# Kernel tuning notes

Hardware: AMD Instinct MI355X
Metric: run time of the kernel (lower is better)

The kernel has to match this reference:

```python
import jax, jax.numpy as jnp
import numpy as np

C = 320        # in_channels == inner_dim (n_heads*d_head = 8*40)
HEADS = 8
DH = 40
CTX = 768
FF_INNER = 1280  # 4*C
G = 32         # GroupNorm groups


def _ln(x, w, b, eps=1e-5):
    m = x.mean(-1, keepdims=True)
    v = ((x - m) ** 2).mean(-1, keepdims=True)
    return (x - m) * jax.lax.rsqrt(v + eps) * w + b


def _attn(q, k, v, heads, scale):
    # faithful to source: split last dim as (d h) -> head index is fastest
    B, Lq, D = q.shape
    Lk = k.shape[1]
    dh = D // heads
    q = q.reshape(B, Lq, dh, heads).transpose(0, 3, 1, 2)  # b h i d
    k = k.reshape(B, Lk, dh, heads).transpose(0, 3, 1, 2)  # b h j d
    v = v.reshape(B, Lk, dh, heads).transpose(0, 3, 1, 2)
    sim = jnp.einsum('bhid,bhjd->bhij', q, k) * scale
    w = jax.nn.softmax(sim, axis=-1)
    o = jnp.einsum('bhij,bhjd->bhid', w, v)
    # merge as (h d): head index is slowest on output (matches source)
    return o.transpose(0, 2, 1, 3).reshape(B, Lq, heads * dh)


def setup_inputs() -> dict:
    key = jax.random.key(0)
    ks = jax.random.split(key, 20)
    n = lambda i, shape: jax.random.normal(ks[i], shape, jnp.float32) * 0.02
    z = lambda d: jnp.zeros((d,), jnp.float32)
    o = lambda d: jnp.ones((d,), jnp.float32)
    return dict(
        x=jax.random.normal(ks[0], (1, C, 64, 64), jnp.float32),
        context=jax.random.normal(ks[1], (1, 77, CTX), jnp.float32),
        gn_w=o(C), gn_b=z(C),
        w_in=n(2, (C, C)), b_in=z(C),
        ln1_w=o(C), ln1_b=z(C),
        wq1=n(3, (C, C)), wk1=n(4, (C, C)), wv1=n(5, (C, C)),
        wo1=n(6, (C, C)), bo1=z(C),
        ln2_w=o(C), ln2_b=z(C),
        wq2=n(7, (C, C)), wk2=n(8, (CTX, C)), wv2=n(9, (CTX, C)),
        wo2=n(10, (C, C)), bo2=z(C),
        ln3_w=o(C), ln3_b=z(C),
        wff1=n(11, (C, 2 * FF_INNER)), bff1=z(2 * FF_INNER),
        wff2=n(12, (FF_INNER, C)), bff2=z(C),
        w_out=n(13, (C, C)), b_out=z(C),
    )


def reference(x, context, gn_w, gn_b, w_in, b_in,
              ln1_w, ln1_b, wq1, wk1, wv1, wo1, bo1,
              ln2_w, ln2_b, wq2, wk2, wv2, wo2, bo2,
              ln3_w, ln3_b, wff1, bff1, wff2, bff2,
              w_out, b_out):
    B, Cc, H, W = x.shape
    scale = DH ** (-0.5)
    x_in = x
    # GroupNorm(32, eps=1e-6)
    g = x.reshape(B, G, Cc // G, H, W)
    m = g.mean((2, 3, 4), keepdims=True)
    v = ((g - m) ** 2).mean((2, 3, 4), keepdims=True)
    h = ((g - m) * jax.lax.rsqrt(v + 1e-6)).reshape(B, Cc, H, W)
    h = h * gn_w[None, :, None, None] + gn_b[None, :, None, None]
    # 1x1 conv in_proj
    h = jnp.einsum('bchw,co->bohw', h, w_in) + b_in[None, :, None, None]
    # b c h w -> b (h w) c
    t = h.transpose(0, 2, 3, 1).reshape(B, H * W, C)
    # --- transformer block (depth=1) ---
    # attn_1: self-attn; NOTE source applies k/v proj to the QUERY projection
    hn = _ln(t, ln1_w, ln1_b)
    q = hn @ wq1
    k = q @ wk1
    vv = q @ wv1
    t = t + (_attn(q, k, vv, HEADS, scale) @ wo1 + bo1)
    # attn_2: cross-attn with context
    hn = _ln(t, ln2_w, ln2_b)
    q = hn @ wq2
    k = context @ wk2
    vv = context @ wv2
    t = t + (_attn(q, k, vv, HEADS, scale) @ wo2 + bo2)
    # GEGLU feed-forward
    hn = _ln(t, ln3_w, ln3_b)
    p = hn @ wff1 + bff1
    a, gate = p[..., :FF_INNER], p[..., FF_INNER:]
    t = t + ((a * jax.nn.gelu(gate, approximate=False)) @ wff2 + bff2)
    # b (h w) c -> b c h w
    s = t.reshape(B, H, W, C).transpose(0, 3, 1, 2)
    out = jnp.einsum('bchw,co->bohw', s, w_out) + b_out[None, :, None, None]
    return out + x_in
```

## Files before the change

### kernel.cpp

```cpp
#include <hip/hip_runtime.h>
#include <hip/hip_bf16.h>
#include <math.h>

#define CCH 320
#define NHEADS 8
#define DH 40
#define HW 4096
#define FFI 1280

typedef __bf16 bf16x8 __attribute__((ext_vector_type(8)));
typedef unsigned short u16x8 __attribute__((ext_vector_type(8)));
typedef short s16x4 __attribute__((ext_vector_type(4)));
typedef float f32x4 __attribute__((ext_vector_type(4)));
typedef unsigned int u32x4 __attribute__((ext_vector_type(4)));

__device__ inline unsigned short f2bf(float f) {
    __hip_bfloat16 h = __float2bfloat16(f);
    return __builtin_bit_cast(unsigned short, h);
}
__device__ inline unsigned pk2bf(float a, float b) {
#if __has_builtin(__builtin_amdgcn_cvt_pk_bf16_f32)
    typedef __bf16 bf16x2 __attribute__((ext_vector_type(2)));
    bf16x2 r = __builtin_amdgcn_cvt_pk_bf16_f32(a, b);
    return __builtin_bit_cast(unsigned, r);
#else
    return (unsigned)f2bf(a) | ((unsigned)f2bf(b) << 16);
#endif
}
__device__ inline float bf2f(unsigned short u) {
    return __builtin_bit_cast(float, ((unsigned)u) << 16);
}
__device__ inline bf16x8 ldfrag(const unsigned short* p) {
    u16x8 raw = *reinterpret_cast<const u16x8*>(p);
    return __builtin_bit_cast(bf16x8, raw);
}
__device__ inline s16x4 pk2frag(unsigned a, unsigned b) {
    unsigned long long v = (unsigned long long)a | ((unsigned long long)b << 32);
    return __builtin_bit_cast(s16x4, v);
}

__device__ inline float ex2(float x) {
#if __has_builtin(__builtin_amdgcn_exp2f)
    return __builtin_amdgcn_exp2f(x);
#else
    return exp2f(x);
#endif
}
__device__ inline float fast_rcp(float x) {
#if __has_builtin(__builtin_amdgcn_rcpf)
    return __builtin_amdgcn_rcpf(x);
#else
    return 1.f / x;
#endif
}
__device__ inline float fast_gelu(float x) {
    float z = fabsf(x) * 0.70710678118654752f;
    float t = fast_rcp(fmaf(0.3275911f, z, 1.f));
    float poly = fmaf(fmaf(fmaf(fmaf(1.061405429f, t, -1.453152027f), t,
                               1.421413741f), t, -0.284496736f), t,
                      0.254829592f) * t;
    float e = ex2(z * z * -1.4426950408889634f);
    float erfz = 1.f - poly * e;
    float s = copysignf(erfz, x);
    return 0.5f * x * (1.f + s);
}

__global__ __launch_bounds__(256) void prep_w2(
    const float* __restrict__ w_in, const float* __restrict__ wq1,
    const float* __restrict__ wk1, const float* __restrict__ wv1,
    const float* __restrict__ wo1, const float* __restrict__ wq2,
    const float* __restrict__ wo2, const float* __restrict__ w_out,
    const float* __restrict__ wff1, const float* __restrict__ wff2,
    const float* __restrict__ wk2, const float* __restrict__ wv2,
    unsigned short* __restrict__ Wt) {
    __shared__ float tile[64][65];
    const int b = blockIdx.x, tid = threadIdx.x;
    const float* src;
    int K, stride, dstoff, k0, n0;
    bool glu = false;
    if (b < 200) {
        int m = b / 25, t = b % 25;
        k0 = (t / 5) * 64; n0 = (t % 5) * 64;
        K = 320; stride = 320; dstoff = m * 102400;
        src = (m == 0) ? w_in : (m == 1) ? wq1 : (m == 2) ? wk1 :
              (m == 3) ? wv1 : (m == 4) ? wo1 : (m == 5) ? wq2 :
              (m == 6) ? wo2 : w_out;
    } else if (b < 300) {
        int t = b - 200;
        k0 = (t / 5) * 64; n0 = (t % 5) * 64;
        K = 1280; stride = 320; dstoff = 1638400; src = wff2;
    } else if (b < 500) {
        int t = b - 300;
        k0 = (t / 40) * 64; n0 = (t % 40) * 64;
        K = 320; stride = 2560; dstoff = 819200; src = wff1; glu = true;
    } else if (b < 560) {
        int t = b - 500;
        k0 = (t / 5) * 64; n0 = (t % 5) * 64;
        K = 768; stride = 320; dstoff = 2048000; src = wk2;
    } else {
        int t = b - 560;
        k0 = (t / 5) * 64; n0 = (t % 5) * 64;
        K = 768; stride = 320; dstoff = 2048000 + 245760; src = wv2;
    }
#pragma unroll
    for (int i = 0; i < 16; ++i) {
        int idx = tid + i * 256;
        int r = idx >> 6, cn = idx & 63;
        int scol = glu ? ((n0 >> 1) + (cn >> 1) + (cn & 1) * FFI) : (n0 + cn);
        tile[r][cn] = src[(size_t)(k0 + r) * stride + scol];
    }
    __syncthreads();
#pragma unroll
    for (int i = 0; i < 16; ++i) {
        int idx = tid + i * 256;
        int cl = idx >> 6, cr = idx & 63;
        Wt[dstoff + (size_t)(n0 + cl) * K + k0 + cr] = f2bf(tile[cr][cl]);
    }
}

__global__ void pack_ctx(const float* __restrict__ ctx,
                         unsigned short* __restrict__ D) {
    int idx = blockIdx.x * 256 + threadIdx.x;
    int row = idx / 768, col = idx - row * 768;
    float v = (row < 77) ? ctx[row * 768 + col] : 0.f;
    D[idx] = f2bf(v);
}

__global__ __launch_bounds__(256) void gn_stats(const float* __restrict__ X,
                                                float2* __restrict__ part) {
    __shared__ float s1[256], s2[256];
    const int b = blockIdx.x, tid = threadIdx.x;
    const float* xg = X + b * 5120;
    float s = 0.f, sq = 0.f;
#pragma unroll
    for (int i = 0; i < 20; ++i) { float v = xg[tid + i * 256]; s += v; sq += v * v; }
    s1[tid] = s; s2[tid] = sq; __syncthreads();
    for (int off = 128; off > 0; off >>= 1) {
        if (tid < off) { s1[tid] += s1[tid + off]; s2[tid] += s2[tid + off]; }
        __syncthreads();
    }
    if (tid == 0) part[b] = make_float2(s1[0], s2[0]);
}

__global__ __launch_bounds__(256) void gn_apply(const float* __restrict__ X,
                                                const float2* __restrict__ part,
                                                const float* __restrict__ w,
                                                const float* __restrict__ b,
                                                unsigned short* __restrict__ Y) {
    __shared__ float tile[64][65];
    __shared__ float gm[32], gr[32];
    const int tid = threadIdx.x;
    const int hw0 = blockIdx.x * 64, c0 = blockIdx.y * 64;
    if (tid < 32) {
        float s = 0.f, sq = 0.f;
#pragma unroll
        for (int i = 0; i < 8; ++i) { float2 p = part[tid * 8 + i]; s += p.x; sq += p.y; }
        float mean = s * (1.f / 40960.f);
        float var  = sq * (1.f / 40960.f) - mean * mean;
        gm[tid] = mean; gr[tid] = rsqrtf(var + 1e-6f);
    }
#pragma unroll
    for (int i = 0; i < 16; ++i) {
        int idx = tid + i * 256;
        int r = idx >> 6, col = idx & 63;
        tile[r][col] = X[(size_t)(c0 + r) * HW + hw0 + col];
    }
    __syncthreads();
#pragma unroll
    for (int i = 0; i < 16; ++i) {
        int idx = tid + i * 256;
        int hwl = idx >> 6, cl = idx & 63;
        int c = c0 + cl, g = c / 10;
        float v = (tile[cl][hwl] - gm[g]) * gr[g] * w[c] + b[c];
        Y[(size_t)(hw0 + hwl) * CCH + c] = f2bf(v);
    }
}

__global__ __launch_bounds__(256) void ln_kernel(const float* __restrict__ X,
                                                 const float* __restrict__ w,
                                                 const float* __restrict__ b,
                                                 unsigned short* __restrict__ Y) {
    const int row  = blockIdx.x * 4 + (threadIdx.x >> 6);
    const int lane = threadIdx.x & 63;
    const float* xr = X + row * CCH;
    const float4 a = *(const float4*)(xr + lane * 4);
    const float  e = xr[256 + lane];
    float v[5] = {a.x, a.y, a.z, a.w, e};
    float s = 0.f, sq = 0.f;
#pragma unroll
    for (int i = 0; i < 5; ++i) { s += v[i]; sq += v[i] * v[i]; }
#pragma unroll
    for (int off = 32; off > 0; off >>= 1) {
        s  += __shfl_xor(s, off, 64);
        sq += __shfl_xor(sq, off, 64);
    }
    const float mean = s * (1.f / 320.f);
    const float var  = sq * (1.f / 320.f) - mean * mean;
    const float rstd = rsqrtf(var + 1e-5f);
    unsigned short* yr = Y + row * CCH;
    const float4 w4 = *(const float4*)(w + lane * 4);
    const float4 b4 = *(const float4*)(b + lane * 4);
    float r0 = (v[0] - mean) * rstd * w4.x + b4.x;
    float r1 = (v[1] - mean) * rstd * w4.y + b4.y;
    float r2 = (v[2] - mean) * rstd * w4.z + b4.z;
    float r3 = (v[3] - mean) * rstd * w4.w + b4.w;
    *(uint2*)(yr + lane * 4) = make_uint2(pk2bf(r0, r1), pk2bf(r2, r3));
    int ct = 256 + lane;
    yr[ct] = f2bf((v[4] - mean) * rstd * w[ct] + b[ct]);
}

template <int MT, int K>
__global__ __launch_bounds__(256) void gemm4(
    const unsigned short* __restrict__ A,
    const unsigned short* __restrict__ Bt,
    const float* __restrict__ bias,
    const float* __restrict__ res,
    void* __restrict__ Cout, void* __restrict__ Cout2,
    int N, int mode, float scale) {
    constexpr int NCH = K / 64;
    __shared__ __align__(16) unsigned short Ab[2][MT * 16 * 64];
    __shared__ __align__(16) unsigned short Bb[2][64 * 64];
    const int tid  = threadIdx.x;
    const int wave = tid >> 6, lane = tid & 63;
    const int quad = lane >> 4, c = lane & 15;
    const int m0 = blockIdx.y * (MT * 16);
    const int bn = blockIdx.x;

    f32x4 acc[MT];
#pragma unroll
    for (int i = 0; i < MT; ++i) acc[i] = (f32x4){0.f, 0.f, 0.f, 0.f};

    const unsigned short* aslab = A + (size_t)m0 * K;
    const unsigned short* bslab = Bt + (size_t)(bn * 64) * K;

    constexpr int ITA = MT * 16 * 8 / 256;
    int arow[ITA], aoff[ITA];
#pragma unroll
    for (int i = 0; i < ITA; ++i) {
        int idx = tid + i * 256;
        arow[i] = idx >> 3;
        int g = idx & 7;
        aoff[i] = arow[i] * 64 + ((g ^ (arow[i] & 7)) * 8);
    }
    int brow[2], boff[2];
#pragma unroll
    for (int i = 0; i < 2; ++i) {
        int idx = tid + i * 256;
        brow[i] = idx >> 3;
        int g = idx & 7;
        boff[i] = brow[i] * 64 + ((g ^ (brow[i] & 7)) * 8);
    }
    const int ag = (tid & 7) * 8;

    {
        u16x8 ra[ITA], rb[2];
#pragma unroll
        for (int i = 0; i < ITA; ++i)
            ra[i] = *(const u16x8*)(aslab + (size_t)arow[i] * K + ag);
#pragma unroll
        for (int i = 0; i < 2; ++i)
            rb[i] = *(const u16x8*)(bslab + (size_t)brow[i] * K + ag);
#pragma unroll
        for (int i = 0; i < ITA; ++i) *(u16x8*)&Ab[0][aoff[i]] = ra[i];
#pragma unroll
        for (int i = 0; i < 2; ++i) *(u16x8*)&Bb[0][boff[i]] = rb[i];
    }
    __syncthreads();

    const int swz0 = (quad ^ (c & 7)) * 8;
    const int swz1 = ((quad + 4) ^ (c & 7)) * 8;
#pragma unroll
    for (int ch = 0; ch < NCH; ++ch) {
        const int buf = ch & 1;
        u16x8 ra[ITA], rb[2];
        if (ch + 1 < NCH) {
            const int kb = (ch + 1) * 64;
#pragma unroll
            for (int i = 0; i < ITA; ++i)
                ra[i] = *(const u16x8*)(aslab + (size_t)arow[i] * K + kb + ag);
#pragma unroll
            for (int i = 0; i < 2; ++i)
                rb[i] = *(const u16x8*)(bslab + (size_t)brow[i] * K + kb + ag);
        }
        bf16x8 b0 = ldfrag(&Bb[buf][(wave * 16 + c) * 64 + swz0]);
        bf16x8 b1 = ldfrag(&Bb[buf][(wave * 16 + c) * 64 + swz1]);
#pragma unroll
        for (int mt = 0; mt < MT; ++mt) {
            bf16x8 a0 = ldfrag(&Ab[buf][(mt * 16 + c) * 64 + swz0]);
            bf16x8 a1 = ldfrag(&Ab[buf][(mt * 16 + c) * 64 + swz1]);
            acc[mt] = __builtin_amdgcn_mfma_f32_16x16x32_bf16(a0, b0, acc[mt], 0, 0, 0);
            acc[mt] = __builtin_amdgcn_mfma_f32_16x16x32_bf16(a1, b1, acc[mt], 0, 0, 0);
        }
        if (ch + 1 < NCH) {
            const int nb = buf ^ 1;
#pragma unroll
            for (int i = 0; i < ITA; ++i) *(u16x8*)&Ab[nb][aoff[i]] = ra[i];
#pragma unroll
            for (int i = 0; i < 2; ++i) *(u16x8*)&Bb[nb][boff[i]] = rb[i];
        }
        __syncthreads();
    }

    const int col = bn * 64 + wave * 16 + c;
    float bval = 0.f;
    if (bias) bval = (mode == 5) ? bias[(col >> 1) + (col & 1) * FFI] : bias[col];

    if (mode == 9) {
#pragma unroll
        for (int mt = 0; mt < MT; ++mt) {
            const int row0 = m0 + mt * 16 + quad * 4;
            float4 xv = *(const float4*)(res + (size_t)col * HW + row0);
            float4 ov;
            ov.x = acc[mt][0] + bval + xv.x;
            ov.y = acc[mt][1] + bval + xv.y;
            ov.z = acc[mt][2] + bval + xv.z;
            ov.w = acc[mt][3] + bval + xv.w;
            *(float4*)((float*)Cout + (size_t)col * HW + row0) = ov;
        }
        return;
    }
#pragma unroll
    for (int mt = 0; mt < MT; ++mt) {
#pragma unroll
        for (int r = 0; r < 4; ++r) {
            const int row = m0 + mt * 16 + quad * 4 + r;
            float v = acc[mt][r];
            if (mode == 0) {
                v += bval;
                if (res) v += res[(size_t)row * N + col];
                ((float*)Cout)[(size_t)row * N + col] = v;
            } else if (mode == 2) {
                int h = col & 7, d = col >> 3;
                ((unsigned short*)Cout)[(((size_t)h << 12) + row) * 64 + d] = f2bf(v * scale);
                if (d < 24)
                    ((unsigned short*)Cout)[(((size_t)h << 12) + row) * 64 + 40 + d] = 0;
            } else if (mode == 4) {
                ((unsigned short*)Cout)[(size_t)row * N + col] =
                    f2bf(v + bval + res[(size_t)row * N + col]);
            } else if (mode == 5) {
                v += bval;
                float other = __shfl_xor(v, 1, 64);
                if ((c & 1) == 0) {
                    float g = fast_gelu(other);
                    ((unsigned short*)Cout)[(size_t)row * FFI + (col >> 1)] = f2bf(v * g);
                }
            } else if (mode == 6) {
                ((unsigned short*)Cout)[(size_t)row * N + col] = f2bf(v);
                int h = col & 7, d = col >> 3;
                ((unsigned short*)Cout2)[(((size_t)h << 12) + row) * 64 + d] = f2bf(v * scale);
                if (d < 24)
                    ((unsigned short*)Cout2)[(((size_t)h << 12) + row) * 64 + 40 + d] = 0;
            } else if (mode == 7) {
                if (col < 320) {
                    int h = col & 7, d = col >> 3;
                    ((unsigned short*)Cout)[(((size_t)h << 12) + row) * 64 + d] = f2bf(v);
                    if (d < 24)
                        ((unsigned short*)Cout)[(((size_t)h << 12) + row) * 64 + 40 + d] = 0;
                } else {
                    int c2 = col - 320;
                    int h = c2 & 7, d = c2 >> 3;
                    ((unsigned short*)Cout2)[(((size_t)(h * 48 + d)) << 12) + row] = f2bf(v);
                    if (d < 8)
                        ((unsigned short*)Cout2)[(((size_t)(h * 48 + 40 + d)) << 12) + row] =
                            (d == 0) ? (unsigned short)0x3F80 : (unsigned short)0;
                }
            } else {
                if (col < 320) {
                    int h = col & 7, d = col >> 3;
                    ((unsigned short*)Cout)[(((size_t)h << 7) + row) * 64 + d] = f2bf(v);
                    if (d < 24)
                        ((unsigned short*)Cout)[(((size_t)h << 7) + row) * 64 + 40 + d] = 0;
                } else {
                    int c2 = col - 320;
                    int h = c2 & 7, d = c2 >> 3;
                    ((unsigned short*)Cout2)[(size_t)(h * 48 + d) * 128 + row] = f2bf(v);
                    if (d < 8)
                        ((unsigned short*)Cout2)[(size_t)(h * 48 + 40 + d) * 128 + row] =
                            (d == 0) ? (unsigned short)0x3F80 : (unsigned short)0;
                }
            }
        }
    }
}

template <int TILES, bool MASK, bool FINAL>
__global__ __launch_bounds__(256) void attn8(
    const unsigned short* __restrict__ Qp,
    const unsigned short* __restrict__ Kp,
    const unsigned short* __restrict__ Vt,
    float* __restrict__ pO, float* __restrict__ pL,
    unsigned short* __restrict__ Ofin,
    int Lk, int Lkp) {
    __shared__ __align__(16) unsigned short Kb[2][64 * 64];
    __shared__ __align__(16) unsigned short Vb[2][48 * 64];
    const int tid  = threadIdx.x;
    const int wave = tid >> 6, lane = tid & 63;
    const int quad = lane >> 4, c = lane & 15;
    const int id  = blockIdx.x;
    const int h   = id & 7;
    const int qt  = (id >> 3) & 31;
    const int seg = id >> 8;
    const int q0  = qt * 128 + wave * 32;

    const unsigned short* qbaseA = Qp + ((((size_t)h << 12) + q0 + c) << 6) + quad * 8;
    const bf16x8 bQA0 = ldfrag(qbaseA);
    const bf16x8 bQA1 = ldfrag(qbaseA + 32);
    const bf16x8 bQB0 = ldfrag(qbaseA + 1024);
    const bf16x8 bQB1 = ldfrag(qbaseA + 1024 + 32);

    f32x4 oA[3], oB[3];
#pragma unroll
    for (int i = 0; i < 3; ++i) {
        oA[i] = (f32x4){0.f, 0.f, 0.f, 0.f};
        oB[i] = (f32x4){0.f, 0.f, 0.f, 0.f};
    }

    const int kt0 = seg * TILES;
    const unsigned short* kglob = Kp + (((size_t)h * Lkp + kt0 * 64) << 6);
    const unsigned short* vglob = Vt + ((size_t)h * 48) * Lkp + kt0 * 64;

    const int r0 = lane >> 3;
    const int g  = lane & 7;
    int ldsoff[4];
    const unsigned short* gptr0[4];
#pragma unroll
    for (int i = 0; i < 4; ++i) {
        int s = wave + 4 * i;
        if (s < 8) {
            int row = s * 8 + r0;
            ldsoff[i] = row * 64 + (g ^ (row & 7)) * 8;
            gptr0[i]  = kglob + (size_t)row * 64 + g * 8;
        } else if (s < 14) {
            int d = (s - 8) * 8 + r0;
            ldsoff[i] = d * 64 + (g ^ (d & 7)) * 8;
            gptr0[i]  = vglob + (size_t)d * Lkp + g * 8;
        } else {
            ldsoff[i] = 0; gptr0[i] = nullptr;
        }
    }
    const bool isK[4] = {(wave + 0) < 8, (wave + 4) < 8, (wave + 8) < 8, (wave + 12) < 8};
    const bool act[4] = {true, true, true, (wave + 12) < 14};

    {
        u16x8 st[4];
#pragma unroll
        for (int i = 0; i < 4; ++i)
            if (act[i]) st[i] = *(const u16x8*)(gptr0[i]);
#pragma unroll
        for (int i = 0; i < 4; ++i)
            if (act[i]) {
                unsigned short* lp = isK[i] ? &Kb[0][ldsoff[i]] : &Vb[0][ldsoff[i]];
                *(u16x8*)lp = st[i];
            }
    }
    __syncthreads();

#pragma unroll
    for (int t = 0; t < TILES; ++t) {
        const int b = t & 1;
        u16x8 st[4];
        if (t + 1 < TILES) {
            const int kb = (t + 1) * 64;
#pragma unroll
            for (int i = 0; i < 4; ++i)
                if (act[i]) {
                    const unsigned short* gp =
                        isK[i] ? (gptr0[i] + (size_t)kb * 64) : (gptr0[i] + kb);
                    st[i] = *(const u16x8*)gp;
                }
        }
        const unsigned short* Kl = &Kb[b][0];
        const unsigned short* Vl = &Vb[b][0];
        const int sw0 = (quad ^ (c & 7)) * 8;
        const int sw1 = ((quad + 4) ^ (c & 7)) * 8;
        f32x4 sA[4], sB[4];
        __builtin_amdgcn_s_setprio(1);
#pragma unroll
        for (int blk = 0; blk < 4; ++blk) {
            const int row = (blk * 16 + c) * 64;
            bf16x8 k0 = ldfrag(Kl + row + sw0);
            bf16x8 k1 = ldfrag(Kl + row + sw1);
            f32x4 zA = {0.f, 0.f, 0.f, 0.f};
            zA = __builtin_amdgcn_mfma_f32_16x16x32_bf16(k0, bQA0, zA, 0, 0, 0);
            zA = __builtin_amdgcn_mfma_f32_16x16x32_bf16(k1, bQA1, zA, 0, 0, 0);
            sA[blk] = zA;
            f32x4 zB = {0.f, 0.f, 0.f, 0.f};
            zB = __builtin_amdgcn_mfma_f32_16x16x32_bf16(k0, bQB0, zB, 0, 0, 0);
            zB = __builtin_amdgcn_mfma_f32_16x16x32_bf16(k1, bQB1, zB, 0, 0, 0);
            sB[blk] = zB;
        }
        __builtin_amdgcn_s_setprio(0);
        if (MASK) {
            const int abs_kb = kt0 * 64 + t * 64;
#pragma unroll
            for (int blk = 0; blk < 4; ++blk)
#pragma unroll
                for (int r = 0; r < 4; ++r) {
                    bool inv = (abs_kb + blk * 16 + quad * 4 + r >= Lk);
                    sA[blk][r] = inv ? -30000.f : sA[blk][r];
                    sB[blk][r] = inv ? -30000.f : sB[blk][r];
                }
        }
        s16x4 PA[4], PB[4];
#pragma unroll
        for (int blk = 0; blk < 4; ++blk) {
            PA[blk] = pk2frag(pk2bf(ex2(sA[blk][0]), ex2(sA[blk][1])),
                              pk2bf(ex2(sA[blk][2]), ex2(sA[blk][3])));
            PB[blk] = pk2frag(pk2bf(ex2(sB[blk][0]), ex2(sB[blk][1])),
                              pk2bf(ex2(sB[blk][2]), ex2(sB[blk][3])));
        }
        __builtin_amdgcn_s_setprio(1);
#pragma unroll
        for (int db = 0; db < 3; ++db) {
            const int dim = db * 16 + c;
            const unsigned short* vrow = Vl + dim * 64;
            const int dswz = dim & 7;
#pragma unroll
            for (int kb = 0; kb < 4; ++kb) {
                const int off = (((kb * 2 + (quad >> 1)) ^ dswz) * 8) + (quad & 1) * 4;
                s16x4 vf = *(const s16x4*)(vrow + off);
                oA[db] = __builtin_amdgcn_mfma_f32_16x16x16bf16_1k(vf, PA[kb], oA[db], 0, 0, 0);
                oB[db] = __builtin_amdgcn_mfma_f32_16x16x16bf16_1k(vf, PB[kb], oB[db], 0, 0, 0);
            }
        }
        __builtin_amdgcn_s_setprio(0);
        if (t + 1 < TILES) {
            const int nb = b ^ 1;
#pragma unroll
            for (int i = 0; i < 4; ++i)
                if (act[i]) {
                    unsigned short* lp = isK[i] ? &Kb[nb][ldsoff[i]] : &Vb[nb][ldsoff[i]];
                    *(u16x8*)lp = st[i];
                }
        }
        __syncthreads();
    }
    if (FINAL) {
        float lA = __shfl(oA[2][0], 32 + c, 64);
        float lB = __shfl(oB[2][0], 32 + c, 64);
        float liA = fast_rcp(lA), liB = fast_rcp(lB);
        unsigned short* oaptr = Ofin + (size_t)(q0 + c) * CCH + h * DH;
        unsigned short* obptr = Ofin + (size_t)(q0 + 16 + c) * CCH + h * DH;
        *(uint2*)(oaptr + quad * 4) =
            make_uint2(pk2bf(oA[0][0] * liA, oA[0][1] * liA),
                       pk2bf(oA[0][2] * liA, oA[0][3] * liA));
        *(uint2*)(oaptr + 16 + quad * 4) =
            make_uint2(pk2bf(oA[1][0] * liA, oA[1][1] * liA),
                       pk2bf(oA[1][2] * liA, oA[1][3] * liA));
        if (quad < 2)
            *(uint2*)(oaptr + 32 + quad * 4) =
                make_uint2(pk2bf(oA[2][0] * liA, oA[2][1] * liA),
                           pk2bf(oA[2][2] * liA, oA[2][3] * liA));
        *(uint2*)(obptr + quad * 4) =
            make_uint2(pk2bf(oB[0][0] * liB, oB[0][1] * liB),
                       pk2bf(oB[0][2] * liB, oB[0][3] * liB));
        *(uint2*)(obptr + 16 + quad * 4) =
            make_uint2(pk2bf(oB[1][0] * liB, oB[1][1] * liB),
                       pk2bf(oB[1][2] * liB, oB[1][3] * liB));
        if (quad < 2)
            *(uint2*)(obptr + 32 + quad * 4) =
                make_uint2(pk2bf(oB[2][0] * liB, oB[2][1] * liB),
                           pk2bf(oB[2][2] * liB, oB[2][3] * liB));
        return;
    }
    const size_t base = ((size_t)(seg * 8 + h)) << 12;
    float* obA = pO + (base + q0 + c) * 40;
    *(float4*)(obA + quad * 4)      = make_float4(oA[0][0], oA[0][1], oA[0][2], oA[0][3]);
    *(float4*)(obA + 16 + quad * 4) = make_float4(oA[1][0], oA[1][1], oA[1][2], oA[1][3]);
    if (quad < 2)
        *(float4*)(obA + 32 + quad * 4) = make_float4(oA[2][0], oA[2][1], oA[2][2], oA[2][3]);
    float* obB = pO + (base + q0 + 16 + c) * 40;
    *(float4*)(obB + quad * 4)      = make_float4(oB[0][0], oB[0][1], oB[0][2], oB[0][3]);
    *(float4*)(obB + 16 + quad * 4) = make_float4(oB[1][0], oB[1][1], oB[1][2], oB[1][3]);
    if (quad < 2)
        *(float4*)(obB + 32 + quad * 4) = make_float4(oB[2][0], oB[2][1], oB[2][2], oB[2][3]);
    if (quad == 2) {
        pL[base + q0 + c]      = oA[2][0];
        pL[base + q0 + 16 + c] = oB[2][0];
    }
}

__global__ __launch_bounds__(256) void attn_combine2(
    const float* __restrict__ pO, const float* __restrict__ pL,
    unsigned short* __restrict__ O, int S) {
    int idx = blockIdx.x * 256 + threadIdx.x;
    int h = idx / (HW * 10);
    int rem = idx - h * (HW * 10);
    int row = rem / 10, dg = rem - row * 10;
    float4 num = make_float4(0.f, 0.f, 0.f, 0.f);
    float den = 0.f;
    for (int s = 0; s < S; ++s) {
        size_t base = ((size_t)(s * 8 + h)) << 12;
        float4 p = *(const float4*)(pO + (base + row) * 40 + dg * 4);
        num.x += p.x; num.y += p.y; num.z += p.z; num.w += p.w;
        den += pL[base + row];
    }
    float inv = fast_rcp(den);
    unsigned short* ob = O + (size_t)row * CCH + h * DH + dg * 4;
    unsigned lo = pk2bf(num.x * inv, num.y * inv);
    unsigned hi = pk2bf(num.z * inv, num.w * inv);
    *(uint2*)ob = make_uint2(lo, hi);
}

extern "C" void kernel_launch(void* const* d_in, const int* in_sizes, int n_in,
                              void* d_out, int out_size, void* d_ws, size_t ws_size,
                              hipStream_t stream) {
    const float* x     = (const float*)d_in[0];
    const float* ctx   = (const float*)d_in[1];
    const float* gn_w  = (const float*)d_in[2];
    const float* gn_b  = (const float*)d_in[3];
    const float* w_in  = (const float*)d_in[4];
    const float* b_in  = (const float*)d_in[5];
    const float* ln1_w = (const float*)d_in[6];
    const float* ln1_b = (const float*)d_in[7];
    const float* wq1   = (const float*)d_in[8];
    const float* wk1   = (const float*)d_in[9];
    const float* wv1   = (const float*)d_in[10];
    const float* wo1   = (const float*)d_in[11];
    const float* bo1   = (const float*)d_in[12];
    const float* ln2_w = (const float*)d_in[13];
    const float* ln2_b = (const float*)d_in[14];
    const float* wq2   = (const float*)d_in[15];
    const float* wk2   = (const float*)d_in[16];
    const float* wv2   = (const float*)d_in[17];
    const float* wo2   = (const float*)d_in[18];
    const float* bo2   = (const float*)d_in[19];
    const float* ln3_w = (const float*)d_in[20];
    const float* ln3_b = (const float*)d_in[21];
    const float* wff1  = (const float*)d_in[22];
    const float* bff1  = (const float*)d_in[23];
    const float* wff2  = (const float*)d_in[24];
    const float* bff2  = (const float*)d_in[25];
    const float* w_out = (const float*)d_in[26];
    const float* b_out = (const float*)d_in[27];
    float* out = (float*)d_out;

    const int NT = HW * CCH;
    float* ws = (float*)d_ws;
    float* t_   = ws;
    float* y_   = t_ + NT;
    float* pO   = y_ + NT;
    float* pL   = pO + 4 * 8 * 4096 * 40;
    float2* gnp = (float2*)(pL + 4 * 8 * 4096);
    unsigned short* u = (unsigned short*)(gnp + 256);
    unsigned short* a_bf = u;                  u += NT;
    unsigned short* q_bf = u;                  u += NT;
    unsigned short* o_bf = u;                  u += NT;
    unsigned short* t_bf = u;                  u += NT;
    unsigned short* g_bf = u;                  u += HW * FFI;
    unsigned short* Qp   = u;                  u += 8 * 4096 * 64;
    unsigned short* Kp   = u;                  u += 8 * 4096 * 64;
    unsigned short* Vt   = u;                  u += 8 * 48 * 4096;
    unsigned short* Kc   = u;                  u += 8 * 128 * 64;
    unsigned short* Vc   = u;                  u += 8 * 48 * 128;
    unsigned short* Wt   = u;                  u += 2048000 + 2 * 245760;
    unsigned short* ctx_bf = u;                u += 128 * 768;

    const unsigned short* w_inT  = Wt;
    const unsigned short* wq1T   = Wt + 102400;
    const unsigned short* wk1T   = Wt + 204800;
    const unsigned short* wo1T   = Wt + 409600;
    const unsigned short* wq2T   = Wt + 512000;
    const unsigned short* wo2T   = Wt + 614400;
    const unsigned short* w_outT = Wt + 716800;
    const unsigned short* wff1T  = Wt + 819200;
    const unsigned short* wff2T  = Wt + 1638400;
    const unsigned short* wk2T   = Wt + 2048000;

    const float qscale = 0.15811388300841897f * 1.4426950408889634f;

    prep_w2<<<620, 256, 0, stream>>>(w_in, wq1, wk1, wv1, wo1, wq2, wo2, w_out,
                                     wff1, wff2, wk2, wv2, Wt);
    pack_ctx<<<384, 256, 0, stream>>>(ctx, ctx_bf);

    gn_stats<<<256, 256, 0, stream>>>(x, gnp);
    gn_apply<<<dim3(64, 5), 256, 0, stream>>>(x, gnp, gn_w, gn_b, a_bf);
    gemm4<2, 320><<<dim3(5, 128), 256, 0, stream>>>(a_bf, w_inT, b_in, nullptr, t_, nullptr, CCH, 0, 1.f);
    ln_kernel<<<1024, 256, 0, stream>>>(t_, ln1_w, ln1_b, a_bf);
    gemm4<2, 320><<<dim3(5, 128), 256, 0, stream>>>(a_bf, wq1T, nullptr, nullptr, q_bf, Qp, CCH, 6, qscale);
    gemm4<4, 320><<<dim3(10, 64), 256, 0, stream>>>(q_bf, wk1T, nullptr, nullptr, Kp, Vt, 640, 7, 1.f);
    attn8<16, false, false><<<1024, 256, 0, stream>>>(Qp, Kp, Vt, pO, pL, nullptr, HW, HW);
    attn_combine2<<<1280, 256, 0, stream>>>(pO, pL, o_bf, 4);
    gemm4<2, 320><<<dim3(5, 128), 256, 0, stream>>>(o_bf, wo1T, bo1, t_, t_, nullptr, CCH, 0, 1.f);
    ln_kernel<<<1024, 256, 0, stream>>>(t_, ln2_w, ln2_b, a_bf);
    gemm4<2, 320><<<dim3(5, 128), 256, 0, stream>>>(a_bf, wq2T, nullptr, nullptr, Qp, nullptr, CCH, 2, qscale);
    gemm4<2, 768><<<dim3(10, 4), 256, 0, stream>>>(ctx_bf, wk2T, nullptr, nullptr, Kc, Vc, 640, 8, 1.f);
    attn8<2, true, true><<<256, 256, 0, stream>>>(Qp, Kc, Vc, nullptr, nullptr, o_bf, 77, 128);
    gemm4<2, 320><<<dim3(5, 128), 256, 0, stream>>>(o_bf, wo2T, bo2, t_, t_, nullptr, CCH, 0, 1.f);
    ln_kernel<<<1024, 256, 0, stream>>>(t_, ln3_w, ln3_b, a_bf);
    gemm4<4, 320><<<dim3(40, 64), 256, 0, stream>>>(a_bf, wff1T, bff1, nullptr, g_bf, nullptr, 2 * FFI, 5, 1.f);
    gemm4<2, 1280><<<dim3(5, 128), 256, 0, stream>>>(g_bf, wff2T, bff2, t_, t_bf, nullptr, CCH, 4, 1.f);
    gemm4<2, 320><<<dim3(5, 128), 256, 0, stream>>>(t_bf, w_outT, b_out, x, out, nullptr, CCH, 9, 1.f);
}
```

Baseline: 304.1 us.

## Interleave attention QK/PV per block and split self-attention keys into more segments

The self-attention inner loop now computes scores, exponentiates and accumulates P·V block by block instead of in three separate phases, and drops the setprio hints. This shortens live ranges and lets MFMA and exp work interleave. Self-attention splits keys into 8 segments (2048 blocks) when the workspace is large enough, and the unused y_ buffer is removed to make room. Two GEMMs switch to smaller row tiles for more blocks. The extra parallelism costs more partial-result traffic in the combine step.

```diff
diff --git a/kernel.cpp b/kernel.cpp
--- a/kernel.cpp
+++ b/kernel.cpp
@@ -473,8 +473,7 @@
         const unsigned short* Vl = &Vb[b][0];
         const int sw0 = (quad ^ (c & 7)) * 8;
         const int sw1 = ((quad + 4) ^ (c & 7)) * 8;
-        f32x4 sA[4], sB[4];
-        __builtin_amdgcn_s_setprio(1);
+        const int abs_kb = kt0 * 64 + t * 64;
 #pragma unroll
         for (int blk = 0; blk < 4; ++blk) {
             const int row = (blk * 16 + c) * 64;
@@ -483,47 +482,31 @@
             f32x4 zA = {0.f, 0.f, 0.f, 0.f};
             zA = __builtin_amdgcn_mfma_f32_16x16x32_bf16(k0, bQA0, zA, 0, 0, 0);
             zA = __builtin_amdgcn_mfma_f32_16x16x32_bf16(k1, bQA1, zA, 0, 0, 0);
-            sA[blk] = zA;
             f32x4 zB = {0.f, 0.f, 0.f, 0.f};
             zB = __builtin_amdgcn_mfma_f32_16x16x32_bf16(k0, bQB0, zB, 0, 0, 0);
             zB = __builtin_amdgcn_mfma_f32_16x16x32_bf16(k1, bQB1, zB, 0, 0, 0);
-            sB[blk] = zB;
-        }
-        __builtin_amdgcn_s_setprio(0);
-        if (MASK) {
-            const int abs_kb = kt0 * 64 + t * 64;
-#pragma unroll
-            for (int blk = 0; blk < 4; ++blk)
+            if (MASK) {
 #pragma unroll
                 for (int r = 0; r < 4; ++r) {
                     bool inv = (abs_kb + blk * 16 + quad * 4 + r >= Lk);
-                    sA[blk][r] = inv ? -30000.f : sA[blk][r];
-                    sB[blk][r] = inv ? -30000.f : sB[blk][r];
+                    zA[r] = inv ? -30000.f : zA[r];
+                    zB[r] = inv ? -30000.f : zB[r];
                 }
-        }
-        s16x4 PA[4], PB[4];
-#pragma unroll
-        for (int blk = 0; blk < 4; ++blk) {
-            PA[blk] = pk2frag(pk2bf(ex2(sA[blk][0]), ex2(sA[blk][1])),
-                              pk2bf(ex2(sA[blk][2]), ex2(sA[blk][3])));
-            PB[blk] = pk2frag(pk2bf(ex2(sB[blk][0]), ex2(sB[blk][1])),
-                              pk2bf(ex2(sB[blk][2]), ex2(sB[blk][3])));
-        }
-        __builtin_amdgcn_s_setprio(1);
-#pragma unroll
-        for (int db = 0; db < 3; ++db) {
-            const int dim = db * 16 + c;
-            const unsigned short* vrow = Vl + dim * 64;
-            const int dswz = dim & 7;
-#pragma unroll
-            for (int kb = 0; kb < 4; ++kb) {
-                const int off = (((kb * 2 + (quad >> 1)) ^ dswz) * 8) + (quad & 1) * 4;
-                s16x4 vf = *(const s16x4*)(vrow + off);
-                oA[db] = __builtin_amdgcn_mfma_f32_16x16x16bf16_1k(vf, PA[kb], oA[db], 0, 0, 0);
-                oB[db] = __builtin_amdgcn_mfma_f32_16x16x16bf16_1k(vf, PB[kb], oB[db], 0, 0, 0);
             }
-        }
-        __builtin_amdgcn_s_setprio(0);
+            s16x4 PA = pk2frag(pk2bf(ex2(zA[0]), ex2(zA[1])),
+                               pk2bf(ex2(zA[2]), ex2(zA[3])));
+            s16x4 PB = pk2frag(pk2bf(ex2(zB[0]), ex2(zB[1])),
+                               pk2bf(ex2(zB[2]), ex2(zB[3])));
+#pragma unroll
+            for (int db = 0; db < 3; ++db) {
+                const int dim = db * 16 + c;
+                const int off =
+                    (((blk * 2 + (quad >> 1)) ^ (dim & 7)) * 8) + (quad & 1) * 4;
+                s16x4 vf = *(const s16x4*)(Vl + dim * 64 + off);
+                oA[db] = __builtin_amdgcn_mfma_f32_16x16x16bf16_1k(vf, PA, oA[db], 0, 0, 0);
+                oB[db] = __builtin_amdgcn_mfma_f32_16x16x16bf16_1k(vf, PB, oB[db], 0, 0, 0);
+            }
+        }
         if (t + 1 < TILES) {
             const int nb = b ^ 1;
 #pragma unroll
@@ -636,12 +619,14 @@
     float* out = (float*)d_out;
 
     const int NT = HW * CCH;
+    const size_t need8 = (size_t)4 * NT * 9 + 8 * 131072 + 2048 + 38010880;
+    const int SEGS = (ws_size >= need8) ? 8 : 4;
+
     float* ws = (float*)d_ws;
     float* t_   = ws;
-    float* y_   = t_ + NT;
-    float* pO   = y_ + NT;
-    float* pL   = pO + 4 * 8 * 4096 * 40;
-    float2* gnp = (float2*)(pL + 4 * 8 * 4096);
+    float* pO   = t_ + NT;
+    float* pL   = pO + (size_t)SEGS * NT;
+    float2* gnp = (float2*)(pL + (size_t)SEGS * 8 * 4096);
     unsigned short* u = (unsigned short*)(gnp + 256);
     unsigned short* a_bf = u;                  u += NT;
     unsigned short* q_bf = u;                  u += NT;
@@ -678,9 +663,12 @@
     gemm4<2, 320><<<dim3(5, 128), 256, 0, stream>>>(a_bf, w_inT, b_in, nullptr, t_, nullptr, CCH, 0, 1.f);
     ln_kernel<<<1024, 256, 0, stream>>>(t_, ln1_w, ln1_b, a_bf);
     gemm4<2, 320><<<dim3(5, 128), 256, 0, stream>>>(a_bf, wq1T, nullptr, nullptr, q_bf, Qp, CCH, 6, qscale);
-    gemm4<4, 320><<<dim3(10, 64), 256, 0, stream>>>(q_bf, wk1T, nullptr, nullptr, Kp, Vt, 640, 7, 1.f);
-    attn8<16, false, false><<<1024, 256, 0, stream>>>(Qp, Kp, Vt, pO, pL, nullptr, HW, HW);
-    attn_combine2<<<1280, 256, 0, stream>>>(pO, pL, o_bf, 4);
+    gemm4<2, 320><<<dim3(10, 128), 256, 0, stream>>>(q_bf, wk1T, nullptr, nullptr, Kp, Vt, 640, 7, 1.f);
+    if (SEGS == 8)
+        attn8<8, false, false><<<2048, 256, 0, stream>>>(Qp, Kp, Vt, pO, pL, nullptr, HW, HW);
+    else
+        attn8<16, false, false><<<1024, 256, 0, stream>>>(Qp, Kp, Vt, pO, pL, nullptr, HW, HW);
+    attn_combine2<<<1280, 256, 0, stream>>>(pO, pL, o_bf, SEGS);
     gemm4<2, 320><<<dim3(5, 128), 256, 0, stream>>>(o_bf, wo1T, bo1, t_, t_, nullptr, CCH, 0, 1.f);
     ln_kernel<<<1024, 256, 0, stream>>>(t_, ln2_w, ln2_b, a_bf);
     gemm4<2, 320><<<dim3(5, 128), 256, 0, stream>>>(a_bf, wq2T, nullptr, nullptr, Qp, nullptr, CCH, 2, qscale);
@@ -688,7 +676,7 @@
     attn8<2, true, true><<<256, 256, 0, stream>>>(Qp, Kc, Vc, nullptr, nullptr, o_bf, 77, 128);
     gemm4<2, 320><<<dim3(5, 128), 256, 0, stream>>>(o_bf, wo2T, bo2, t_, t_, nullptr, CCH, 0, 1.f);
     ln_kernel<<<1024, 256, 0, stream>>>(t_, ln3_w, ln3_b, a_bf);
-    gemm4<4, 320><<<dim3(40, 64), 256, 0, stream>>>(a_bf, wff1T, bff1, nullptr, g_bf, nullptr, 2 * FFI, 5, 1.f);
+    gemm4<2, 320><<<dim3(40, 128), 256, 0, stream>>>(a_bf, wff1T, bff1, nullptr, g_bf, nullptr, 2 * FFI, 5, 1.f);
     gemm4<2, 1280><<<dim3(5, 128), 256, 0, stream>>>(g_bf, wff2T, bff2, t_, t_bf, nullptr, CCH, 4, 1.f);
     gemm4<2, 320><<<dim3(5, 128), 256, 0, stream>>>(t_bf, w_outT, b_out, x, out, nullptr, CCH, 9, 1.f);
 }
```

Result: no change. 301.0 us (-1.0%).
